# Performance work log

Measured on AMD Instinct MI355X. Metric: run time of the kernel, lower is better.

Reference implementation:

```python
import jax, jax.numpy as jnp
import numpy as np

N = 21  # nodes per graph (20 laser sectors + 1 robot node)
MAX_RANGE = 10.0
_bound = np.linspace(-np.pi / 2 - 0.03, np.pi / 2, 21, dtype=np.float32)[:-1]
_angles = _bound + np.float32(np.pi / 20)
ANGLE_FEAT = jnp.asarray(np.stack([np.sin(_angles), np.cos(_angles)], 1), dtype=jnp.float32)  # [20,2]


def _build_nodes(state24):
    # state24: [B,24] -> node features [B,21,7]
    B = state24.shape[0]
    laser = state24[:, :20, None] / MAX_RANGE                       # [B,20,1]
    angle = jnp.broadcast_to(ANGLE_FEAT[None], (B, 20, 2))          # [B,20,2]
    sector = jnp.concatenate([laser, angle, jnp.zeros((B, 20, 4), state24.dtype)], -1)  # [B,20,7]
    robot = jnp.concatenate([jnp.zeros((B, 1, 3), state24.dtype), state24[:, None, 20:]], -1)  # [B,1,7]
    return jnp.concatenate([sector, robot], axis=1)                 # [B,21,7]


def _gatv2(x, Wl, Wr, att, bias, heads, dim):
    # GATv2 over a fully-connected graph with self-loops (dense all-pairs).
    # e_ij = att . leaky_relu(Wl x_j + Wr x_i); alpha = softmax_j; out_i = sum_j alpha_ij (Wl x_j)
    B = x.shape[0]
    gl = (x @ Wl).reshape(B, N, heads, dim)  # source transform [B,j,H,D]
    gr = (x @ Wr).reshape(B, N, heads, dim)  # target transform [B,i,H,D]
    s = jax.nn.leaky_relu(gl[:, None] + gr[:, :, None], negative_slope=0.2)  # [B,i,j,H,D]
    e = jnp.einsum('bijhd,hd->bijh', s, att)                                  # [B,i,j,H]
    alpha = jax.nn.softmax(e, axis=2)                                          # softmax over sources j
    out = jnp.einsum('bijh,bjhd->bihd', alpha, gl).reshape(B, N, heads * dim)
    return out + bias


def setup_inputs() -> dict:
    key = jax.random.key(0)
    ks = jax.random.split(key, 16)
    r = lambda k, shape, s: (jax.random.normal(k, shape, dtype=jnp.float32) * s)
    B = 1024
    return {
        'state24': jax.random.normal(ks[0], (B, 24), dtype=jnp.float32),
        'Wl1': r(ks[1], (7, 256), 0.3), 'Wr1': r(ks[2], (7, 256), 0.3),
        'att1': r(ks[3], (4, 64), 0.1), 'b1': r(ks[4], (256,), 0.02),
        'Wl2': r(ks[5], (256, 64), 0.06), 'Wr2': r(ks[6], (256, 64), 0.06),
        'att2': r(ks[7], (1, 64), 0.1), 'b2': r(ks[8], (64,), 0.02),
        'fc1_w': r(ks[9], (64, 256), 0.12), 'fc1_b': r(ks[10], (256,), 0.02),
        'fc2_w': r(ks[11], (256, 256), 0.06), 'fc2_b': r(ks[12], (256,), 0.02),
        'fc3_w': r(ks[13], (256, 2), 0.06), 'fc3_b': r(ks[14], (2,), 0.02),
    }


def reference(state24, Wl1, Wr1, att1, b1, Wl2, Wr2, att2, b2,
              fc1_w, fc1_b, fc2_w, fc2_b, fc3_w, fc3_b):
    x = _build_nodes(state24)                               # [B,21,7]
    h = jax.nn.elu(_gatv2(x, Wl1, Wr1, att1, b1, 4, 64))    # [B,21,256]
    h = _gatv2(h, Wl2, Wr2, att2, b2, 1, 64)                # [B,21,64]
    nfv = jnp.mean(h, axis=1)                               # global_mean_pool -> [B,64]
    h = jax.nn.relu(nfv @ fc1_w + fc1_b)
    h = jax.nn.relu(h @ fc2_w + fc2_b)
    return jnp.tanh(h @ fc3_w + fc3_b)                      # [B,2]
```

## Files before the change

### kernel.cpp

```cpp
#include <hip/hip_runtime.h>
#include <hip/hip_fp16.h>
#include <math.h>

#define PI_D 3.141592653589793

typedef _Float16 h2 __attribute__((ext_vector_type(2)));
typedef _Float16 h8 __attribute__((ext_vector_type(8)));
typedef unsigned short us8 __attribute__((ext_vector_type(8)));
typedef __fp16 f16v2 __attribute__((ext_vector_type(2)));

#define STR1 264
#define STR1O 33
#define STR2 66
#define EPS 24

static __device__ __forceinline__ h2 pack_h2(float a, float b) {
    return __builtin_bit_cast(h2, __builtin_amdgcn_cvt_pkrtz(a, b));
}

static __device__ __forceinline__ float fdot2(h2 a, h2 b, float c) {
    return __builtin_amdgcn_fdot2(__builtin_bit_cast(f16v2, a),
                                  __builtin_bit_cast(f16v2, b), c, false);
}

static __device__ __forceinline__ h8 habs8(h8 x) {
    us8 u = __builtin_bit_cast(us8, x);
    us8 m = {0x7fff, 0x7fff, 0x7fff, 0x7fff, 0x7fff, 0x7fff, 0x7fff, 0x7fff};
    return __builtin_bit_cast(h8, (us8)(u & m));
}

__global__ __launch_bounds__(256) void pack_weights_kernel(
    const float* __restrict__ Wl2, const float* __restrict__ Wr2,
    const float* __restrict__ fc1_w, const float* __restrict__ fc2_w,
    h8* __restrict__ ws)
{
    int idx = blockIdx.x * 256 + threadIdx.x;
    if (idx < 4096) {
        const float* W = idx < 2048 ? Wl2 : Wr2;
        int t = idx & 2047;
        int ch = t >> 6, c = t & 63;
        h8 o;
        #pragma unroll
        for (int r = 0; r < 8; ++r) o[r] = (_Float16)W[(8 * ch + r) * 64 + c];
        ws[idx] = o;
    } else if (idx < 6144) {
        int t = idx - 4096;
        int k2 = t >> 6, c = t & 63;
        h8 o;
        #pragma unroll
        for (int q = 0; q < 4; ++q) {
            o[2 * q]     = (_Float16)fc1_w[(2 * k2) * 256 + 4 * c + q];
            o[2 * q + 1] = (_Float16)fc1_w[(2 * k2 + 1) * 256 + 4 * c + q];
        }
        ws[idx] = o;
    } else {
        int t = idx - 6144;
        int k2 = t >> 6, c = t & 63;
        h8 o;
        #pragma unroll
        for (int q = 0; q < 4; ++q) {
            o[2 * q]     = (_Float16)fc2_w[(2 * k2) * 256 + 4 * c + q];
            o[2 * q + 1] = (_Float16)fc2_w[(2 * k2 + 1) * 256 + 4 * c + q];
        }
        ws[idx] = o;
    }
}

__global__ __launch_bounds__(256, 4) void actor_fused_kernel(
    const float* __restrict__ state24,
    const float* __restrict__ Wl1, const float* __restrict__ Wr1,
    const float* __restrict__ att1, const float* __restrict__ b1,
    const float* __restrict__ att2, const float* __restrict__ b2,
    const float* __restrict__ fc1_b, const float* __restrict__ fc2_b,
    const float* __restrict__ fc3_w, const float* __restrict__ fc3_b,
    const h8* __restrict__ wsL, const h8* __restrict__ wsR,
    const h8* __restrict__ wsF1, const h8* __restrict__ wsF2,
    float* __restrict__ out, int B)
{
    const int bix = blockIdx.x;
    if (bix >= B) return;
    const int tid = threadIdx.x;

    __shared__ float sinL[20], cosL[20], laserL[20], robotL[4];
    __shared__ __align__(16) h2 attLh[128];
    __shared__ __align__(16) float att2L[64];
    __shared__ __align__(16) _Float16 gr1h[24 * STR1];
    __shared__ __align__(16) union {
        struct { _Float16 gl1h[21 * STR1];
                 float eP[84 * EPS];
                 float uv[168]; } p1;
        struct { float gl2[24 * STR2]; float gr2[24 * STR2]; float e2[504];
                 float red[4][256];
                 _Float16 nfvh[64]; _Float16 hah[256]; _Float16 hbh[256]; } p2;
    } U;

    if (tid < 20) {
        double step = (PI_D + 0.03) / 20.0;
        float bound = (float)(-PI_D / 2.0 - 0.03 + (double)tid * step);
        float ang = bound + (float)(PI_D / 20.0);
        sinL[tid] = sinf(ang);
        cosL[tid] = cosf(ang);
        laserL[tid] = state24[bix * 24 + tid] * 0.1f;
    }
    if (tid >= 32 && tid < 36) robotL[tid - 32] = state24[bix * 24 + 20 + (tid - 32)];
    if (tid < 128) {
        float2 ap = ((const float2*)att1)[tid];
        attLh[tid] = pack_h2(ap.x, ap.y);
    }
    if (tid < 64) att2L[tid] = att2[tid];
    __syncthreads();

    {
        float wl[7], wr[7];
        #pragma unroll
        for (int k = 0; k < 7; k++) { wl[k] = Wl1[k * 256 + tid]; wr[k] = Wr1[k * 256 + tid]; }
        #pragma unroll
        for (int n = 0; n < 20; n++) {
            float l = laserL[n], s = sinL[n], c = cosL[n];
            U.p1.gl1h[n * STR1 + tid] = (_Float16)(l * wl[0] + s * wl[1] + c * wl[2]);
            gr1h[n * STR1 + tid]     = (_Float16)(l * wr[0] + s * wr[1] + c * wr[2]);
        }
        float r0 = robotL[0], r1 = robotL[1], r2 = robotL[2], r3 = robotL[3];
        U.p1.gl1h[20 * STR1 + tid] = (_Float16)(r0 * wl[3] + r1 * wl[4] + r2 * wl[5] + r3 * wl[6]);
        gr1h[20 * STR1 + tid]     = (_Float16)(r0 * wr[3] + r1 * wr[4] + r2 * wr[5] + r3 * wr[6]);
    }
    __syncthreads();

    if (tid < 168) {
        int r = tid < 84 ? tid : tid - 84;
        int h = r / 21, idx = r - h * 21;
        const _Float16* rowp = (tid < 84 ? U.p1.gl1h : gr1h) + idx * STR1 + h * 64;
        const h8* row8 = (const h8*)rowp;
        const h2* ar = attLh + h * 32;
        float l0 = 0.f, l1 = 0.f;
        #pragma unroll
        for (int ch = 0; ch < 8; ++ch) {
            h8 g = row8[ch];
            l0 = fdot2(__builtin_shufflevector(g, g, 0, 1), ar[ch * 4 + 0], l0);
            l1 = fdot2(__builtin_shufflevector(g, g, 2, 3), ar[ch * 4 + 1], l1);
            l0 = fdot2(__builtin_shufflevector(g, g, 4, 5), ar[ch * 4 + 2], l0);
            l1 = fdot2(__builtin_shufflevector(g, g, 6, 7), ar[ch * 4 + 3], l1);
        }
        U.p1.uv[tid] = l0 + l1;
    }
    __syncthreads();

    {
        const int h = tid >> 6;
        const int lane = tid & 63;
        h2 ar[32];
        #pragma unroll
        for (int q = 0; q < 32; ++q) ar[q] = attLh[h * 32 + q];
        const float* uvU = U.p1.uv + h * 21;
        const float* uvV = U.p1.uv + 84 + h * 21;

        for (int it = 0; it < 7; ++it) {
            int q = it * 64 + lane;
            if (q < 441) {
                int i = q / 21;
                int j = q - i * 21;
                const h8* gA8 = (const h8*)(U.p1.gl1h + j * STR1 + h * 64);
                const h8* gB8 = (const h8*)(gr1h + i * STR1 + h * 64);
                float m0 = 0.f, m1 = 0.f;
                #pragma unroll
                for (int ch = 0; ch < 8; ++ch) {
                    h8 x = gA8[ch] + gB8[ch];
                    h8 ax = habs8(x);
                    m0 = fdot2(__builtin_shufflevector(ax, ax, 0, 1), ar[ch * 4 + 0], m0);
                    m1 = fdot2(__builtin_shufflevector(ax, ax, 2, 3), ar[ch * 4 + 1], m1);
                    m0 = fdot2(__builtin_shufflevector(ax, ax, 4, 5), ar[ch * 4 + 2], m0);
                    m1 = fdot2(__builtin_shufflevector(ax, ax, 6, 7), ar[ch * 4 + 3], m1);
                }
                U.p1.eP[(h * 21 + i) * EPS + j] = 0.6f * (uvU[j] + uvV[i]) + 0.4f * (m0 + m1);
            }
        }
    }
    __syncthreads();

    if (tid < 84) {
        float* row = U.p1.eP + tid * EPS;
        float m = row[0];
        #pragma unroll
        for (int j = 1; j < 21; j++) m = fmaxf(m, row[j]);
        float s = 0.f;
        #pragma unroll
        for (int j = 0; j < 21; j++) { float v = __expf(row[j] - m); row[j] = v; s += v; }
        float r = 1.f / s;
        #pragma unroll
        for (int j = 0; j < 21; j++) row[j] *= r;
    }
    __syncthreads();

    {
        const int h = tid >> 6, c = tid & 63;
        const int col = h * 64 + c;
        float glv[21];
        #pragma unroll
        for (int j = 0; j < 21; ++j) glv[j] = (float)U.p1.gl1h[j * STR1 + col];
        float bb = b1[col];
        gr1h[21 * STR1 + col] = (_Float16)0.f;
        gr1h[22 * STR1 + col] = (_Float16)0.f;
        gr1h[23 * STR1 + col] = (_Float16)0.f;
        for (int i = 0; i < 21; ++i) {
            const float4* ar4 = (const float4*)(U.p1.eP + (h * 21 + i) * EPS);
            float4 q0 = ar4[0], q1 = ar4[1], q2 = ar4[2], q3 = ar4[3], q4 = ar4[4];
            float a20 = U.p1.eP[(h * 21 + i) * EPS + 20];
            float acc;
            acc = q0.x * glv[0];
            acc = fmaf(q0.y, glv[1], acc);
            acc = fmaf(q0.z, glv[2], acc);
            acc = fmaf(q0.w, glv[3], acc);
            acc = fmaf(q1.x, glv[4], acc);
            acc = fmaf(q1.y, glv[5], acc);
            acc = fmaf(q1.z, glv[6], acc);
            acc = fmaf(q1.w, glv[7], acc);
            acc = fmaf(q2.x, glv[8], acc);
            acc = fmaf(q2.y, glv[9], acc);
            acc = fmaf(q2.z, glv[10], acc);
            acc = fmaf(q2.w, glv[11], acc);
            acc = fmaf(q3.x, glv[12], acc);
            acc = fmaf(q3.y, glv[13], acc);
            acc = fmaf(q3.z, glv[14], acc);
            acc = fmaf(q3.w, glv[15], acc);
            acc = fmaf(q4.x, glv[16], acc);
            acc = fmaf(q4.y, glv[17], acc);
            acc = fmaf(q4.z, glv[18], acc);
            acc = fmaf(q4.w, glv[19], acc);
            acc = fmaf(a20, glv[20], acc);
            float v = acc + bb;
            v = v > 0.f ? v : __expf(v) - 1.f;
            gr1h[i * STR1 + col] = (_Float16)v;
        }
    }
    __syncthreads();

    {
        int c = tid & 63, g = tid >> 6;
        float accL[6] = {0, 0, 0, 0, 0, 0}, accR[6] = {0, 0, 0, 0, 0, 0};
        const h8* hrow8 = (const h8*)gr1h;
        for (int ch = 0; ch < 32; ++ch) {
            h8 wl = wsL[ch * 64 + c];
            h8 wr = wsR[ch * 64 + c];
            h2 wlA = __builtin_shufflevector(wl, wl, 0, 1);
            h2 wlB = __builtin_shufflevector(wl, wl, 2, 3);
            h2 wlC = __builtin_shufflevector(wl, wl, 4, 5);
            h2 wlD = __builtin_shufflevector(wl, wl, 6, 7);
            h2 wrA = __builtin_shufflevector(wr, wr, 0, 1);
            h2 wrB = __builtin_shufflevector(wr, wr, 2, 3);
            h2 wrC = __builtin_shufflevector(wr, wr, 4, 5);
            h2 wrD = __builtin_shufflevector(wr, wr, 6, 7);
            #pragma unroll
            for (int m = 0; m < 6; ++m) {
                int n = g + 4 * m;
                h8 hv = hrow8[n * STR1O + ch];
                h2 s0 = __builtin_shufflevector(hv, hv, 0, 1);
                h2 s1 = __builtin_shufflevector(hv, hv, 2, 3);
                h2 s2 = __builtin_shufflevector(hv, hv, 4, 5);
                h2 s3 = __builtin_shufflevector(hv, hv, 6, 7);
                accL[m] = fdot2(s0, wlA, accL[m]);
                accL[m] = fdot2(s1, wlB, accL[m]);
                accL[m] = fdot2(s2, wlC, accL[m]);
                accL[m] = fdot2(s3, wlD, accL[m]);
                accR[m] = fdot2(s0, wrA, accR[m]);
                accR[m] = fdot2(s1, wrB, accR[m]);
                accR[m] = fdot2(s2, wrC, accR[m]);
                accR[m] = fdot2(s3, wrD, accR[m]);
            }
        }
        #pragma unroll
        for (int m = 0; m < 6; ++m) {
            int n = g + 4 * m;
            U.p2.gl2[n * STR2 + c] = accL[m];
            U.p2.gr2[n * STR2 + c] = accR[m];
        }
    }
    __syncthreads();

    for (int it = 0; it < 2; ++it) {
        int t = it * 256 + tid;
        if (t < 441) {
            int i = t / 21;
            int j = t - i * 21;
            const float2* gA = (const float2*)(U.p2.gl2 + j * STR2);
            const float2* gB = (const float2*)(U.p2.gr2 + i * STR2);
            const float2* aa = (const float2*)att2L;
            float l0 = 0.f, l1 = 0.f, m0 = 0.f, m1 = 0.f;
            #pragma unroll
            for (int dp = 0; dp < 32; ++dp) {
                float2 va = gA[dp], vb = gB[dp], a = aa[dp];
                float x0 = va.x + vb.x, x1 = va.y + vb.y;
                l0 = fmaf(a.x, x0, l0); m0 = fmaf(a.x, fabsf(x0), m0);
                l1 = fmaf(a.y, x1, l1); m1 = fmaf(a.y, fabsf(x1), m1);
            }
            U.p2.e2[t] = 0.6f * (l0 + l1) + 0.4f * (m0 + m1);
        }
    }
    __syncthreads();

    if (tid < 24) {
        float* row = U.p2.e2 + tid * 21;
        if (tid < 21) {
            float m = row[0];
            #pragma unroll
            for (int j = 1; j < 21; j++) m = fmaxf(m, row[j]);
            float s = 0.f;
            #pragma unroll
            for (int j = 0; j < 21; j++) { float v = __expf(row[j] - m); row[j] = v; s += v; }
            float r = 1.f / s;
            #pragma unroll
            for (int j = 0; j < 21; j++) row[j] *= r;
        } else {
            #pragma unroll
            for (int j = 0; j < 21; j++) row[j] = 0.f;
        }
    }
    __syncthreads();

    {
        int d = tid & 63, g = tid >> 6;
        float sacc = 0.f;
        #pragma unroll
        for (int m = 0; m < 6; ++m) {
            int i = g + 4 * m;
            const float* al = U.p2.e2 + i * 21;
            float acc = 0.f;
            #pragma unroll
            for (int j = 0; j < 21; ++j) acc = fmaf(al[j], U.p2.gl2[j * STR2 + d], acc);
            sacc += acc;
        }
        U.p2.red[g][d] = sacc;
    }
    __syncthreads();
    if (tid < 64) {
        float v = (U.p2.red[0][tid] + U.p2.red[1][tid] + U.p2.red[2][tid] + U.p2.red[3][tid])
                  * (1.f / 21.f) + b2[tid];
        U.p2.nfvh[tid] = (_Float16)v;
    }
    __syncthreads();

    {
        int c = tid & 63, g = tid >> 6;
        const h2* x2p = (const h2*)U.p2.nfvh;
        float4 acc = {0.f, 0.f, 0.f, 0.f};
        #pragma unroll
        for (int kk = 0; kk < 8; ++kk) {
            int k2 = g * 8 + kk;
            h8 w = wsF1[k2 * 64 + c];
            h2 x2 = x2p[k2];
            acc.x = fdot2(__builtin_shufflevector(w, w, 0, 1), x2, acc.x);
            acc.y = fdot2(__builtin_shufflevector(w, w, 2, 3), x2, acc.y);
            acc.z = fdot2(__builtin_shufflevector(w, w, 4, 5), x2, acc.z);
            acc.w = fdot2(__builtin_shufflevector(w, w, 6, 7), x2, acc.w);
        }
        ((float4*)U.p2.red[g])[c] = acc;
    }
    __syncthreads();
    {
        float v = U.p2.red[0][tid] + U.p2.red[1][tid] + U.p2.red[2][tid] + U.p2.red[3][tid]
                  + fc1_b[tid];
        U.p2.hah[tid] = (_Float16)fmaxf(v, 0.f);
    }
    __syncthreads();

    {
        int c = tid & 63, g = tid >> 6;
        const h8* haH = (const h8*)U.p2.hah;
        float4 acc = {0.f, 0.f, 0.f, 0.f};
#define FC2_STEP(q, p)                                                          \
        {                                                                       \
            int k2 = g * 32 + (q) * 4 + (p);                                    \
            h8 w = wsF2[k2 * 64 + c];                                           \
            h2 x2 = __builtin_shufflevector(xa, xa, 2 * (p), 2 * (p) + 1);      \
            acc.x = fdot2(__builtin_shufflevector(w, w, 0, 1), x2, acc.x);      \
            acc.y = fdot2(__builtin_shufflevector(w, w, 2, 3), x2, acc.y);      \
            acc.z = fdot2(__builtin_shufflevector(w, w, 4, 5), x2, acc.z);      \
            acc.w = fdot2(__builtin_shufflevector(w, w, 6, 7), x2, acc.w);      \
        }
        #pragma unroll
        for (int q = 0; q < 8; ++q) {
            h8 xa = haH[g * 8 + q];
            FC2_STEP(q, 0)
            FC2_STEP(q, 1)
            FC2_STEP(q, 2)
            FC2_STEP(q, 3)
        }
#undef FC2_STEP
        ((float4*)U.p2.red[g])[c] = acc;
    }
    __syncthreads();
    {
        float v = U.p2.red[0][tid] + U.p2.red[1][tid] + U.p2.red[2][tid] + U.p2.red[3][tid]
                  + fc2_b[tid];
        U.p2.hbh[tid] = (_Float16)fmaxf(v, 0.f);
    }
    __syncthreads();

    if (tid < 128) {
        int o = tid >> 6, l = tid & 63;
        float s = 0.f;
        #pragma unroll
        for (int m = 0; m < 4; m++) {
            int k = l + 64 * m;
            s = fmaf((float)U.p2.hbh[k], fc3_w[k * 2 + o], s);
        }
        #pragma unroll
        for (int off = 32; off >= 1; off >>= 1) s += __shfl_down(s, off, 64);
        if (l == 0) out[bix * 2 + o] = tanhf(s + fc3_b[o]);
    }
}

extern "C" void kernel_launch(void* const* d_in, const int* in_sizes, int n_in,
                              void* d_out, int out_size, void* d_ws, size_t ws_size,
                              hipStream_t stream) {
    const float* state24 = (const float*)d_in[0];
    const float* Wl1 = (const float*)d_in[1];
    const float* Wr1 = (const float*)d_in[2];
    const float* att1 = (const float*)d_in[3];
    const float* b1 = (const float*)d_in[4];
    const float* Wl2 = (const float*)d_in[5];
    const float* Wr2 = (const float*)d_in[6];
    const float* att2 = (const float*)d_in[7];
    const float* b2 = (const float*)d_in[8];
    const float* fc1_w = (const float*)d_in[9];
    const float* fc1_b = (const float*)d_in[10];
    const float* fc2_w = (const float*)d_in[11];
    const float* fc2_b = (const float*)d_in[12];
    const float* fc3_w = (const float*)d_in[13];
    const float* fc3_b = (const float*)d_in[14];
    float* out = (float*)d_out;

    h8* ws = (h8*)d_ws;
    const h8* wsL = ws;
    const h8* wsR = ws + 2048;
    const h8* wsF1 = ws + 4096;
    const h8* wsF2 = ws + 6144;

    pack_weights_kernel<<<56, 256, 0, stream>>>(Wl2, Wr2, fc1_w, fc2_w, ws);

    int B = in_sizes[0] / 24;
    actor_fused_kernel<<<B, 256, 0, stream>>>(
        state24, Wl1, Wr1, att1, b1, att2, b2,
        fc1_b, fc2_b, fc3_w, fc3_b,
        wsL, wsR, wsF1, wsF2, out, B);
}
```

Baseline: 130.5 us.

## Use MFMA 16x16x32 f16 for second GATv2 layer projections

Replaces the per-thread fdot2 loops that compute the layer-2 source and target projections with MFMA 16x16x32 f16 instructions. Each wave computes a 16-column tile for two 16-row M tiles. The weight packing kernel is changed to the MFMA B-operand lane layout. The hidden-state buffer is padded to 32 rows with zero fill. This adds shared memory use, which could reduce occupancy.

```diff
diff --git a/kernel.cpp b/kernel.cpp
--- a/kernel.cpp
+++ b/kernel.cpp
@@ -8,9 +8,10 @@
 typedef _Float16 h8 __attribute__((ext_vector_type(8)));
 typedef unsigned short us8 __attribute__((ext_vector_type(8)));
 typedef __fp16 f16v2 __attribute__((ext_vector_type(2)));
+typedef __fp16 f16v8 __attribute__((ext_vector_type(8)));
+typedef float f32x4 __attribute__((ext_vector_type(4)));
 
 #define STR1 264
-#define STR1O 33
 #define STR2 66
 #define EPS 24
 
@@ -27,6 +28,11 @@
     us8 u = __builtin_bit_cast(us8, x);
     us8 m = {0x7fff, 0x7fff, 0x7fff, 0x7fff, 0x7fff, 0x7fff, 0x7fff, 0x7fff};
     return __builtin_bit_cast(h8, (us8)(u & m));
+}
+
+static __device__ __forceinline__ f32x4 mfma16(h8 a, h8 b, f32x4 c) {
+    return __builtin_amdgcn_mfma_f32_16x16x32_f16(
+        __builtin_bit_cast(f16v8, a), __builtin_bit_cast(f16v8, b), c, 0, 0, 0);
 }
 
 __global__ __launch_bounds__(256) void pack_weights_kernel(
@@ -38,10 +44,13 @@
     if (idx < 4096) {
         const float* W = idx < 2048 ? Wl2 : Wr2;
         int t = idx & 2047;
-        int ch = t >> 6, c = t & 63;
+        int ntile = t >> 9, rem = t & 511;
+        int kchunk = rem >> 6, lane = rem & 63;
+        int n = ntile * 16 + (lane & 15);
+        int k0 = kchunk * 32 + (lane >> 4) * 8;
         h8 o;
         #pragma unroll
-        for (int r = 0; r < 8; ++r) o[r] = (_Float16)W[(8 * ch + r) * 64 + c];
+        for (int j = 0; j < 8; ++j) o[j] = (_Float16)W[(k0 + j) * 64 + n];
         ws[idx] = o;
     } else if (idx < 6144) {
         int t = idx - 4096;
@@ -84,7 +93,7 @@
     __shared__ float sinL[20], cosL[20], laserL[20], robotL[4];
     __shared__ __align__(16) h2 attLh[128];
     __shared__ __align__(16) float att2L[64];
-    __shared__ __align__(16) _Float16 gr1h[24 * STR1];
+    __shared__ __align__(16) _Float16 gr1h[32 * STR1];
     __shared__ __align__(16) union {
         struct { _Float16 gl1h[21 * STR1];
                  float eP[84 * EPS];
@@ -192,15 +201,17 @@
     __syncthreads();
 
     {
+        h8* z8 = (h8*)gr1h;
+        h8 zz = {(_Float16)0.f, (_Float16)0.f, (_Float16)0.f, (_Float16)0.f,
+                 (_Float16)0.f, (_Float16)0.f, (_Float16)0.f, (_Float16)0.f};
+        for (int z = tid; z < 363; z += 256) z8[693 + z] = zz;
+
         const int h = tid >> 6, c = tid & 63;
         const int col = h * 64 + c;
         float glv[21];
         #pragma unroll
         for (int j = 0; j < 21; ++j) glv[j] = (float)U.p1.gl1h[j * STR1 + col];
         float bb = b1[col];
-        gr1h[21 * STR1 + col] = (_Float16)0.f;
-        gr1h[22 * STR1 + col] = (_Float16)0.f;
-        gr1h[23 * STR1 + col] = (_Float16)0.f;
         for (int i = 0; i < 21; ++i) {
             const float4* ar4 = (const float4*)(U.p1.eP + (h * 21 + i) * EPS);
             float4 q0 = ar4[0], q1 = ar4[1], q2 = ar4[2], q3 = ar4[3], q4 = ar4[4];
@@ -235,43 +246,38 @@
     __syncthreads();
 
     {
-        int c = tid & 63, g = tid >> 6;
-        float accL[6] = {0, 0, 0, 0, 0, 0}, accR[6] = {0, 0, 0, 0, 0, 0};
-        const h8* hrow8 = (const h8*)gr1h;
-        for (int ch = 0; ch < 32; ++ch) {
-            h8 wl = wsL[ch * 64 + c];
-            h8 wr = wsR[ch * 64 + c];
-            h2 wlA = __builtin_shufflevector(wl, wl, 0, 1);
-            h2 wlB = __builtin_shufflevector(wl, wl, 2, 3);
-            h2 wlC = __builtin_shufflevector(wl, wl, 4, 5);
-            h2 wlD = __builtin_shufflevector(wl, wl, 6, 7);
-            h2 wrA = __builtin_shufflevector(wr, wr, 0, 1);
-            h2 wrB = __builtin_shufflevector(wr, wr, 2, 3);
-            h2 wrC = __builtin_shufflevector(wr, wr, 4, 5);
-            h2 wrD = __builtin_shufflevector(wr, wr, 6, 7);
-            #pragma unroll
-            for (int m = 0; m < 6; ++m) {
-                int n = g + 4 * m;
-                h8 hv = hrow8[n * STR1O + ch];
-                h2 s0 = __builtin_shufflevector(hv, hv, 0, 1);
-                h2 s1 = __builtin_shufflevector(hv, hv, 2, 3);
-                h2 s2 = __builtin_shufflevector(hv, hv, 4, 5);
-                h2 s3 = __builtin_shufflevector(hv, hv, 6, 7);
-                accL[m] = fdot2(s0, wlA, accL[m]);
-                accL[m] = fdot2(s1, wlB, accL[m]);
-                accL[m] = fdot2(s2, wlC, accL[m]);
-                accL[m] = fdot2(s3, wlD, accL[m]);
-                accR[m] = fdot2(s0, wrA, accR[m]);
-                accR[m] = fdot2(s1, wrB, accR[m]);
-                accR[m] = fdot2(s2, wrC, accR[m]);
-                accR[m] = fdot2(s3, wrD, accR[m]);
+        const int lane = tid & 63;
+        const int w = tid >> 6;
+        const int mrow = lane & 15;
+        const int quad = lane >> 4;
+        const h8* hA0 = (const h8*)(gr1h + mrow * STR1 + quad * 8);
+        const h8* hA1 = (const h8*)(gr1h + (16 + mrow) * STR1 + quad * 8);
+        const h8* bL = wsL + w * 512 + lane;
+        const h8* bR = wsR + w * 512 + lane;
+        f32x4 aL0 = {0.f, 0.f, 0.f, 0.f}, aL1 = {0.f, 0.f, 0.f, 0.f};
+        f32x4 aR0 = {0.f, 0.f, 0.f, 0.f}, aR1 = {0.f, 0.f, 0.f, 0.f};
+        #pragma unroll
+        for (int kc = 0; kc < 8; ++kc) {
+            h8 A0 = hA0[kc * 4];
+            h8 A1 = hA1[kc * 4];
+            h8 BL = bL[kc * 64];
+            h8 BR = bR[kc * 64];
+            aL0 = mfma16(A0, BL, aL0);
+            aL1 = mfma16(A1, BL, aL1);
+            aR0 = mfma16(A0, BR, aR0);
+            aR1 = mfma16(A1, BR, aR1);
+        }
+        const int col = w * 16 + mrow;
+        #pragma unroll
+        for (int r = 0; r < 4; ++r) {
+            int row0 = quad * 4 + r;
+            U.p2.gl2[row0 * STR2 + col] = aL0[r];
+            U.p2.gr2[row0 * STR2 + col] = aR0[r];
+            int row1 = 16 + row0;
+            if (row1 < 24) {
+                U.p2.gl2[row1 * STR2 + col] = aL1[r];
+                U.p2.gr2[row1 * STR2 + col] = aR1[r];
             }
-        }
-        #pragma unroll
-        for (int m = 0; m < 6; ++m) {
-            int n = g + 4 * m;
-            U.p2.gl2[n * STR2 + c] = accL[m];
-            U.p2.gr2[n * STR2 + c] = accR[m];
         }
     }
     __syncthreads();
```

New measurement: 117.6 us. -9.9%, faster.
